# Kernel tuning notes

Hardware: AMD Instinct MI355X
Metric: run time of the kernel (lower is better)

Reference implementation:

```python
import jax, jax.numpy as jnp
import numpy as np

B, L, D, H = 2, 2048, 1024, 16
HD = D // H  # head_dim = 64


def setup_inputs() -> dict:
    key = jax.random.key(0)
    ks = jax.random.split(key, 10)
    s_in = 1.0 / np.sqrt(D)
    x = jax.random.normal(ks[0], (B, L, D), dtype=jnp.float32)
    attn_mask = jnp.ones((B, L), dtype=jnp.int32)
    # Per-head QKV projections stacked along head axis: (H, D, HD)
    Wq = jax.random.normal(ks[1], (H, D, HD), dtype=jnp.float32) * s_in
    bq = jnp.zeros((H, HD), dtype=jnp.float32)
    Wk = jax.random.normal(ks[2], (H, D, HD), dtype=jnp.float32) * s_in
    bk = jnp.zeros((H, HD), dtype=jnp.float32)
    Wv = jax.random.normal(ks[3], (H, D, HD), dtype=jnp.float32) * s_in
    bv = jnp.zeros((H, HD), dtype=jnp.float32)
    # Output projection (D, D)
    Wo = jax.random.normal(ks[4], (D, D), dtype=jnp.float32) * s_in
    bo = jnp.zeros((D,), dtype=jnp.float32)
    return {"x": x, "attn_mask": attn_mask, "Wq": Wq, "bq": bq,
            "Wk": Wk, "bk": bk, "Wv": Wv, "bv": bv, "Wo": Wo, "bo": bo}


def reference(x, attn_mask, Wq, bq, Wk, bk, Wv, bv, Wo, bo):
    # Batched equivalent of the per-head loop: q,k,v -> (B, H, L, HD)
    q = jnp.einsum('bld,hde->bhle', x, Wq) + bq[None, :, None, :]
    k = jnp.einsum('bld,hde->bhle', x, Wk) + bk[None, :, None, :]
    v = jnp.einsum('bld,hde->bhle', x, Wv) + bv[None, :, None, :]
    scale = 1.0 / jnp.sqrt(jnp.asarray(HD, dtype=x.dtype))
    scores = jnp.einsum('bhle,bhme->bhlm', q, k) * scale  # (B, H, L, L)
    # attn_mask (B, L): mask out keys where mask == 0
    neg = jnp.asarray(-1e9, dtype=scores.dtype)
    scores = jnp.where(attn_mask[:, None, None, :] != 0, scores, neg)
    attn = jax.nn.softmax(scores, axis=-1)
    ctx = jnp.einsum('bhlm,bhme->bhle', attn, v)  # (B, H, L, HD)
    # Concatenate heads (head h occupies dims [h*HD:(h+1)*HD]) then project
    concat = jnp.transpose(ctx, (0, 2, 1, 3)).reshape(B, L, D)
    out = jnp.einsum('bld,de->ble', concat, Wo) + bo
    return out
```

## Files before the change

kernel.cpp:

```cpp
#include <hip/hip_runtime.h>

constexpr int Bz = 2, Lz = 2048, Dz = 1024, Hz = 16, HDz = 64;
constexpr int QSZ = Bz * Hz * Lz * HDz;
constexpr int SPLIT = 2;
constexpr int KSPAN = Lz / SPLIT;

typedef __attribute__((ext_vector_type(8))) __bf16 bf16x8;
typedef __attribute__((ext_vector_type(4))) float f32x4;

__device__ __forceinline__ float b2f(unsigned int u) {
    union { float f; unsigned int i; } c; c.i = u << 16; return c.f;
}
__device__ __forceinline__ unsigned short f2b(float x) {
    union { float f; unsigned int u; } c; c.f = x;
    unsigned int u = c.u;
    return (unsigned short)((u + 0x7fffu + ((u >> 16) & 1u)) >> 16);
}
__device__ __forceinline__ void ld8(const float* p, float* f) {
    float4 a = *(const float4*)p, b = *(const float4*)(p + 4);
    f[0] = a.x; f[1] = a.y; f[2] = a.z; f[3] = a.w;
    f[4] = b.x; f[5] = b.y; f[6] = b.z; f[7] = b.w;
}
__device__ __forceinline__ int swb(int row, int e) {
    return row * 64 + ((((e >> 3) ^ row) & 7) << 3) + (e & 7);
}

__global__ void ws_sentinel(float* __restrict__ out) {
    if (threadIdx.x == 0 && blockIdx.x == 0) out[0] = 100.0f;
}

__global__ __launch_bounds__(256) void cvt_x(
    const float* __restrict__ x, unsigned short* __restrict__ xb) {
    int idx = (blockIdx.x * 256 + threadIdx.x) * 8;
    float f[8]; ld8(x + idx, f);
    union { unsigned short s[8]; uint4 u; } o;
    #pragma unroll
    for (int j = 0; j < 8; ++j) o.s[j] = f2b(f[j]);
    *(uint4*)(xb + idx) = o.u;
}

__global__ __launch_bounds__(256) void cvt_w(
    const float* __restrict__ Wq, const float* __restrict__ Wk,
    const float* __restrict__ Wv, const float* __restrict__ Wo,
    unsigned short* __restrict__ Wt, unsigned short* __restrict__ Wot) {
    const int tid = threadIdx.x;
    const int z = blockIdx.z;
    const int kseg = blockIdx.x * 4 + (tid >> 6);
    const int k0 = kseg * 16;
    unsigned short o[16];
    if (z < 3) {
        const float* W = (z == 0) ? Wq : (z == 1) ? Wk : Wv;
        const int h = blockIdx.y, n = tid & 63;
        const float* src = W + (size_t)h * Dz * HDz;
        #pragma unroll
        for (int j = 0; j < 16; ++j) o[j] = f2b(src[(size_t)(k0 + j) * HDz + n]);
        unsigned short* dst = Wt + ((size_t)((z * Hz + h) * HDz) + n) * Dz + k0;
        *(uint4*)dst = *(uint4*)o;
        *(uint4*)(dst + 8) = *(uint4*)(o + 8);
    } else {
        const int n = blockIdx.y * 64 + (tid & 63);
        #pragma unroll
        for (int j = 0; j < 16; ++j) o[j] = f2b(Wo[(size_t)(k0 + j) * Dz + n]);
        unsigned short* dst = Wot + (size_t)n * Dz + k0;
        *(uint4*)dst = *(uint4*)o;
        *(uint4*)(dst + 8) = *(uint4*)(o + 8);
    }
}

__global__ __launch_bounds__(256) void qkv_mfma(
    const unsigned short* __restrict__ xb, const unsigned short* __restrict__ Wt,
    const float* __restrict__ bq, const float* __restrict__ bk,
    const float* __restrict__ bv, unsigned short* __restrict__ qkv) {
    const int l0 = blockIdx.x * 256;
    const int h = blockIdx.y;
    const int which = blockIdx.z % 3;
    const int b = blockIdx.z / 3;
    const float* bias = (which == 0) ? bq : (which == 1) ? bk : bv;
    const int tid = threadIdx.x, wave = tid >> 6, lane = tid & 63;
    const int quad = lane >> 4, l16 = lane & 15;

    __shared__ __align__(16) unsigned short As[256 * 64];
    __shared__ __align__(16) unsigned short Bs[64 * 64];

    const unsigned short* xrow = xb + (size_t)(b * Lz + l0) * Dz;
    const unsigned short* wbase = Wt + (size_t)((which * Hz + h) * HDz) * Dz;

    f32x4 acc[4][4];
    #pragma unroll
    for (int mi = 0; mi < 4; ++mi)
        #pragma unroll
        for (int ni = 0; ni < 4; ++ni) acc[mi][ni] = (f32x4){0.f, 0.f, 0.f, 0.f};

    for (int t = 0; t < Dz / 64; ++t) {
        const int k0 = t * 64;
        #pragma unroll
        for (int i = 0; i < 8; ++i) {
            int ci = tid + i * 256;
            int row = ci >> 3, c = ci & 7;
            uint4 u = *(const uint4*)(xrow + (size_t)row * Dz + k0 + c * 8);
            *(uint4*)&As[row * 64 + ((c ^ (row & 7)) << 3)] = u;
        }
        #pragma unroll
        for (int i = 0; i < 2; ++i) {
            int ci = tid + i * 256;
            int n = ci >> 3, c = ci & 7;
            uint4 u = *(const uint4*)(wbase + (size_t)n * Dz + k0 + c * 8);
            *(uint4*)&Bs[n * 64 + ((c ^ (n & 7)) << 3)] = u;
        }
        __syncthreads();
        #pragma unroll
        for (int kh = 0; kh < 2; ++kh) {
            bf16x8 a[4], bb[4];
            #pragma unroll
            for (int mi = 0; mi < 4; ++mi)
                a[mi] = *(const bf16x8*)&As[swb(wave * 64 + mi * 16 + l16, kh * 32 + quad * 8)];
            #pragma unroll
            for (int ni = 0; ni < 4; ++ni)
                bb[ni] = *(const bf16x8*)&Bs[swb(ni * 16 + l16, kh * 32 + quad * 8)];
            #pragma unroll
            for (int mi = 0; mi < 4; ++mi)
                #pragma unroll
                for (int ni = 0; ni < 4; ++ni)
                    acc[mi][ni] = __builtin_amdgcn_mfma_f32_16x16x32_bf16(
                        a[mi], bb[ni], acc[mi][ni], 0, 0, 0);
        }
        __syncthreads();
    }
    unsigned short* outp = qkv + (size_t)which * QSZ + ((size_t)(b * Hz + h) * Lz + l0) * HDz;
    #pragma unroll
    for (int ni = 0; ni < 4; ++ni) {
        float bvv = bias[h * HDz + ni * 16 + l16];
        #pragma unroll
        for (int mi = 0; mi < 4; ++mi)
            #pragma unroll
            for (int r = 0; r < 4; ++r) {
                int row = wave * 64 + mi * 16 + quad * 4 + r;
                outp[(size_t)row * HDz + ni * 16 + l16] = f2b(acc[mi][ni][r] + bvv);
            }
    }
}

__global__ __launch_bounds__(256) void attn_mfma(
    const unsigned short* __restrict__ qkv, const int* __restrict__ mask,
    unsigned short* __restrict__ Opart, float* __restrict__ lsb) {
    const int b = blockIdx.z >> 1, split = blockIdx.z & 1;
    const int h = blockIdx.y, qb = blockIdx.x;
    const int wave = threadIdx.x >> 6, lane = threadIdx.x & 63;
    const int quad = lane >> 4, l16 = lane & 15;
    const unsigned short* Q = qkv + (size_t)((b * Hz + h) * Lz) * HDz;
    const unsigned short* K = Q + QSZ;
    const unsigned short* V = Q + 2 * (size_t)QSZ;

    __shared__ __align__(16) unsigned short Ks[64 * 64];
    __shared__ __align__(16) unsigned short Vt[64 * 64];
    __shared__ __align__(16) unsigned short Pw[4][32 * 64];

    const int row0 = qb * 128 + wave * 32;
    bf16x8 aq[2][2];
    #pragma unroll
    for (int s = 0; s < 2; ++s) {
        const unsigned short* qp = Q + (size_t)(row0 + s * 16 + l16) * HDz;
        aq[s][0] = *(const bf16x8*)(qp + quad * 8);
        aq[s][1] = *(const bf16x8*)(qp + 32 + quad * 8);
    }

    f32x4 O[2][4];
    #pragma unroll
    for (int s = 0; s < 2; ++s)
        #pragma unroll
        for (int nc = 0; nc < 4; ++nc) O[s][nc] = (f32x4){0.f, 0.f, 0.f, 0.f};
    float lacc[2] = {0.f, 0.f};

    const int vp = threadIdx.x & 31, vc = threadIdx.x >> 5;

    for (int t = 0; t < KSPAN / 64; ++t) {
        const int kt0 = split * KSPAN + t * 64;
        #pragma unroll
        for (int i = 0; i < 2; ++i) {
            int ci = threadIdx.x + i * 256;
            int key = ci >> 3, c = ci & 7;
            uint4 u = *(const uint4*)(K + (size_t)(kt0 + key) * HDz + c * 8);
            *(uint4*)&Ks[key * 64 + ((c ^ (key & 7)) << 3)] = u;
        }
        {
            const unsigned short* vsrc = V + (size_t)(kt0 + 2 * vp) * HDz + vc * 8;
            uint4 u0 = *(const uint4*)vsrc;
            uint4 u1 = *(const uint4*)(vsrc + HDz);
            unsigned short a0[8], a1[8];
            *(uint4*)a0 = u0; *(uint4*)a1 = u1;
            unsigned int* Vt32 = (unsigned int*)Vt;
            #pragma unroll
            for (int j = 0; j < 8; ++j) {
                int row = vc * 8 + j;
                Vt32[row * 32 + ((((vp >> 2) ^ (row & 7)) << 2) + (vp & 3))] =
                    (unsigned int)a0[j] | ((unsigned int)a1[j] << 16);
            }
        }
        unsigned long long bal = __ballot(mask[b * Lz + kt0 + lane] != 0);
        bool allv = (bal == ~0ull);
        __syncthreads();

        float sh[4][4];
        if (allv) {
            #pragma unroll
            for (int kc = 0; kc < 4; ++kc)
                #pragma unroll
                for (int r = 0; r < 4; ++r) sh[kc][r] = -12.0f;
        } else {
            #pragma unroll
            for (int kc = 0; kc < 4; ++kc)
                #pragma unroll
                for (int r = 0; r < 4; ++r)
                    sh[kc][r] = mask[b * Lz + kt0 + kc * 16 + quad * 4 + r] ? -12.0f : -1e9f;
        }

        unsigned short* Pme = Pw[wave];
        #pragma unroll
        for (int kc = 0; kc < 4; ++kc) {
            bf16x8 aK0 = *(const bf16x8*)&Ks[swb(kc * 16 + l16, quad * 8)];
            bf16x8 aK1 = *(const bf16x8*)&Ks[swb(kc * 16 + l16, 32 + quad * 8)];
            #pragma unroll
            for (int s = 0; s < 2; ++s) {
                f32x4 sv = (f32x4){0.f, 0.f, 0.f, 0.f};
                sv = __builtin_amdgcn_mfma_f32_16x16x32_bf16(aK0, aq[s][0], sv, 0, 0, 0);
                sv = __builtin_amdgcn_mfma_f32_16x16x32_bf16(aK1, aq[s][1], sv, 0, 0, 0);
                float p[4];
                #pragma unroll
                for (int r = 0; r < 4; ++r)
                    p[r] = __expf(fmaf(sv[r], 0.125f, sh[kc][r]));
                lacc[s] += (p[0] + p[1]) + (p[2] + p[3]);
                uint2 pk;
                pk.x = (unsigned int)f2b(p[0]) | ((unsigned int)f2b(p[1]) << 16);
                pk.y = (unsigned int)f2b(p[2]) | ((unsigned int)f2b(p[3]) << 16);
                *(uint2*)&Pme[swb(s * 16 + l16, kc * 16 + quad * 4)] = pk;
            }
        }
        #pragma unroll
        for (int kc2 = 0; kc2 < 2; ++kc2) {
            bf16x8 aP0 = *(const bf16x8*)&Pme[swb(l16, kc2 * 32 + quad * 8)];
            bf16x8 aP1 = *(const bf16x8*)&Pme[swb(16 + l16, kc2 * 32 + quad * 8)];
            #pragma unroll
            for (int nc = 0; nc < 4; ++nc) {
                bf16x8 bV = *(const bf16x8*)&Vt[swb(nc * 16 + l16, kc2 * 32 + quad * 8)];
                O[0][nc] = __builtin_amdgcn_mfma_f32_16x16x32_bf16(aP0, bV, O[0][nc], 0, 0, 0);
                O[1][nc] = __builtin_amdgcn_mfma_f32_16x16x32_bf16(aP1, bV, O[1][nc], 0, 0, 0);
            }
        }
        __syncthreads();
    }
    #pragma unroll
    for (int s = 0; s < 2; ++s) {
        lacc[s] += __shfl_xor(lacc[s], 16, 64);
        lacc[s] += __shfl_xor(lacc[s], 32, 64);
    }
    const size_t rowbase = (size_t)(b * Hz + h) * Lz + row0;
    if (quad == 0) {
        atomicAdd(&lsb[rowbase + l16], lacc[0]);
        atomicAdd(&lsb[rowbase + 16 + l16], lacc[1]);
    }
    unsigned short* Os = Opart + (size_t)split * QSZ + rowbase * HDz - (size_t)row0 * HDz
                         + (size_t)row0 * HDz;
    #pragma unroll
    for (int s = 0; s < 2; ++s)
        #pragma unroll
        for (int r = 0; r < 4; ++r) {
            int row = s * 16 + quad * 4 + r;
            #pragma unroll
            for (int nc = 0; nc < 4; ++nc)
                Os[(size_t)row * HDz + nc * 16 + l16] = f2b(O[s][nc][r]);
        }
}

__global__ __launch_bounds__(256) void combine(
    const unsigned short* __restrict__ Opart, const float* __restrict__ lsb,
    unsigned short* __restrict__ ctx) {
    int idx8 = (blockIdx.x * 256 + threadIdx.x) * 8;
    float inv = 1.0f / lsb[idx8 >> 6];
    uint4 u0 = *(const uint4*)(Opart + idx8);
    uint4 u1 = *(const uint4*)(Opart + QSZ + idx8);
    unsigned short a0[8], a1[8], o[8];
    *(uint4*)a0 = u0; *(uint4*)a1 = u1;
    #pragma unroll
    for (int j = 0; j < 8; ++j)
        o[j] = f2b((b2f(a0[j]) + b2f(a1[j])) * inv);
    *(uint4*)(ctx + idx8) = *(uint4*)o;
}

__global__ __launch_bounds__(256) void out_mfma(
    const unsigned short* __restrict__ ctx, const unsigned short* __restrict__ Wot,
    const float* __restrict__ bo, float* __restrict__ out) {
    const int r0 = blockIdx.x * 128;
    const int n0 = blockIdx.y * 64;
    const int b = r0 >> 11, lbase = r0 & 2047;
    const int tid = threadIdx.x, wave = tid >> 6, lane = tid & 63;
    const int quad = lane >> 4, l16 = lane & 15;

    __shared__ __align__(16) unsigned short As[128 * 64];
    __shared__ __align__(16) unsigned short Bs[64 * 64];

    f32x4 acc[2][4];
    #pragma unroll
    for (int mi = 0; mi < 2; ++mi)
        #pragma unroll
        for (int ni = 0; ni < 4; ++ni) acc[mi][ni] = (f32x4){0.f, 0.f, 0.f, 0.f};

    for (int t = 0; t < Hz; ++t) {
        const unsigned short* abase = ctx + ((size_t)(b * Hz + t) * Lz + lbase) * HDz;
        #pragma unroll
        for (int i = 0; i < 4; ++i) {
            int ci = tid + i * 256;
            int row = ci >> 3, c = ci & 7;
            uint4 u = *(const uint4*)(abase + (size_t)row * HDz + c * 8);
            *(uint4*)&As[row * 64 + ((c ^ (row & 7)) << 3)] = u;
        }
        #pragma unroll
        for (int i = 0; i < 2; ++i) {
            int ci = tid + i * 256;
            int n = ci >> 3, c = ci & 7;
            uint4 u = *(const uint4*)(Wot + (size_t)(n0 + n) * Dz + t * 64 + c * 8);
            *(uint4*)&Bs[n * 64 + ((c ^ (n & 7)) << 3)] = u;
        }
        __syncthreads();
        #pragma unroll
        for (int kh = 0; kh < 2; ++kh) {
            bf16x8 a[2], bb[4];
            #pragma unroll
            for (int mi = 0; mi < 2; ++mi)
                a[mi] = *(const bf16x8*)&As[swb(wave * 32 + mi * 16 + l16, kh * 32 + quad * 8)];
            #pragma unroll
            for (int ni = 0; ni < 4; ++ni)
                bb[ni] = *(const bf16x8*)&Bs[swb(ni * 16 + l16, kh * 32 + quad * 8)];
            #pragma unroll
            for (int mi = 0; mi < 2; ++mi)
                #pragma unroll
                for (int ni = 0; ni < 4; ++ni)
                    acc[mi][ni] = __builtin_amdgcn_mfma_f32_16x16x32_bf16(
                        a[mi], bb[ni], acc[mi][ni], 0, 0, 0);
        }
        __syncthreads();
    }
    #pragma unroll
    for (int ni = 0; ni < 4; ++ni) {
        float bvv = bo[n0 + ni * 16 + l16];
        #pragma unroll
        for (int mi = 0; mi < 2; ++mi)
            #pragma unroll
            for (int r = 0; r < 4; ++r) {
                int row = r0 + wave * 32 + mi * 16 + quad * 4 + r;
                out[(size_t)row * Dz + n0 + ni * 16 + l16] = acc[mi][ni][r] + bvv;
            }
    }
}

extern "C" void kernel_launch(void* const* d_in, const int* in_sizes, int n_in,
                              void* d_out, int out_size, void* d_ws, size_t ws_size,
                              hipStream_t stream) {
    const float* x    = (const float*)d_in[0];
    const int*   mask = (const int*)d_in[1];
    const float* Wq = (const float*)d_in[2];
    const float* bq = (const float*)d_in[3];
    const float* Wk = (const float*)d_in[4];
    const float* bk = (const float*)d_in[5];
    const float* Wv = (const float*)d_in[6];
    const float* bv = (const float*)d_in[7];
    const float* Wo = (const float*)d_in[8];
    const float* bo = (const float*)d_in[9];
    float* out = (float*)d_out;

    const size_t WT_E  = (size_t)3 * Hz * HDz * Dz;
    const size_t WOT_E = (size_t)Dz * Dz;
    const size_t LS_E  = (size_t)Bz * Hz * Lz;
    const size_t NEED = 256 + ((size_t)3 * QSZ + WT_E + WOT_E) * sizeof(unsigned short)
                        + LS_E * sizeof(float);
    if (ws_size < NEED) {
        ws_sentinel<<<1, 64, 0, stream>>>(out);
        return;
    }
    unsigned short* qkv = (unsigned short*)((char*)d_ws + 256);
    unsigned short* Wt  = qkv + (size_t)3 * QSZ;
    unsigned short* Wot = Wt + WT_E;
    float* lsb = (float*)(Wot + WOT_E);
    unsigned short* xb    = (unsigned short*)d_out;
    unsigned short* Opart = (unsigned short*)d_out;

    hipMemsetAsync(lsb, 0, LS_E * sizeof(float), stream);
    cvt_x<<<(Bz * Lz * Dz) / (256 * 8), 256, 0, stream>>>(x, xb);
    cvt_w<<<dim3(16, 16, 4), 256, 0, stream>>>(Wq, Wk, Wv, Wo, Wt, Wot);
    qkv_mfma<<<dim3(Lz / 256, Hz, Bz * 3), 256, 0, stream>>>(xb, Wt, bq, bk, bv, qkv);
    attn_mfma<<<dim3(Lz / 128, Hz, Bz * SPLIT), 256, 0, stream>>>(qkv, mask, Opart, lsb);
    combine<<<QSZ / (256 * 8), 256, 0, stream>>>(Opart, lsb, qkv);
    out_mfma<<<dim3((Bz * Lz) / 128, Dz / 64), 256, 0, stream>>>(qkv, Wot, bo, out);
}
```

Measured before the change: 230.0 us.

## Fuse prep kernels, retile QKV GEMM to 128x128, use hardware bf16 packing

Merges the x conversion, weight conversion and lsb memset into a single prep launch to cut launch overhead. Retiles the QKV projection as one GEMM over all 3*H*HD output columns with 128x128 tiles and a 2x2 wave layout, scattering results into the per-head q/k/v layout at store time. This improves operand reuse per tile and changes the grid shape. It also replaces the manual float-to-bf16 rounding with native bf16x2 conversions in several kernels, which may round slightly differently on edge cases.

```diff
diff --git a/kernel.cpp b/kernel.cpp
--- a/kernel.cpp
+++ b/kernel.cpp
@@ -6,6 +6,7 @@
 constexpr int KSPAN = Lz / SPLIT;
 
 typedef __attribute__((ext_vector_type(8))) __bf16 bf16x8;
+typedef __attribute__((ext_vector_type(2))) __bf16 bf16x2;
 typedef __attribute__((ext_vector_type(4))) float f32x4;
 
 __device__ __forceinline__ float b2f(unsigned int u) {
@@ -16,6 +17,11 @@
     unsigned int u = c.u;
     return (unsigned short)((u + 0x7fffu + ((u >> 16) & 1u)) >> 16);
 }
+__device__ __forceinline__ unsigned int pkbf(float a, float b) {
+    union { bf16x2 v; unsigned int u; } c;
+    c.v = (bf16x2){(__bf16)a, (__bf16)b};
+    return c.u;
+}
 __device__ __forceinline__ void ld8(const float* p, float* f) {
     float4 a = *(const float4*)p, b = *(const float4*)(p + 4);
     f[0] = a.x; f[1] = a.y; f[2] = a.z; f[3] = a.w;
@@ -29,41 +35,46 @@
     if (threadIdx.x == 0 && blockIdx.x == 0) out[0] = 100.0f;
 }
 
-__global__ __launch_bounds__(256) void cvt_x(
-    const float* __restrict__ x, unsigned short* __restrict__ xb) {
-    int idx = (blockIdx.x * 256 + threadIdx.x) * 8;
-    float f[8]; ld8(x + idx, f);
-    union { unsigned short s[8]; uint4 u; } o;
-    #pragma unroll
-    for (int j = 0; j < 8; ++j) o.s[j] = f2b(f[j]);
-    *(uint4*)(xb + idx) = o.u;
-}
-
-__global__ __launch_bounds__(256) void cvt_w(
+__global__ __launch_bounds__(256) void prep(
+    const float* __restrict__ x,
     const float* __restrict__ Wq, const float* __restrict__ Wk,
     const float* __restrict__ Wv, const float* __restrict__ Wo,
-    unsigned short* __restrict__ Wt, unsigned short* __restrict__ Wot) {
-    const int tid = threadIdx.x;
-    const int z = blockIdx.z;
-    const int kseg = blockIdx.x * 4 + (tid >> 6);
-    const int k0 = kseg * 16;
-    unsigned short o[16];
-    if (z < 3) {
-        const float* W = (z == 0) ? Wq : (z == 1) ? Wk : Wv;
-        const int h = blockIdx.y, n = tid & 63;
-        const float* src = W + (size_t)h * Dz * HDz;
-        #pragma unroll
-        for (int j = 0; j < 16; ++j) o[j] = f2b(src[(size_t)(k0 + j) * HDz + n]);
-        unsigned short* dst = Wt + ((size_t)((z * Hz + h) * HDz) + n) * Dz + k0;
-        *(uint4*)dst = *(uint4*)o;
-        *(uint4*)(dst + 8) = *(uint4*)(o + 8);
+    unsigned short* __restrict__ xb, unsigned short* __restrict__ Wt,
+    unsigned short* __restrict__ Wot, float* __restrict__ lsb) {
+    const int bid = blockIdx.x, tid = threadIdx.x;
+    if (bid < 2048) {
+        int idx = (bid * 256 + tid) * 8;
+        float f[8]; ld8(x + idx, f);
+        unsigned int o[4];
+        #pragma unroll
+        for (int j = 0; j < 4; ++j) o[j] = pkbf(f[2 * j], f[2 * j + 1]);
+        *(uint4*)(xb + idx) = *(uint4*)o;
+    } else if (bid < 2048 + 1024) {
+        int zz = bid - 2048;
+        int z = zz >> 8, y = (zz >> 4) & 15, xk = zz & 15;
+        int kseg = xk * 4 + (tid >> 6);
+        int k0 = kseg * 16;
+        unsigned short o[16];
+        if (z < 3) {
+            const float* W = (z == 0) ? Wq : (z == 1) ? Wk : Wv;
+            const int h = y, n = tid & 63;
+            const float* src = W + (size_t)h * Dz * HDz;
+            #pragma unroll
+            for (int j = 0; j < 16; ++j) o[j] = f2b(src[(size_t)(k0 + j) * HDz + n]);
+            unsigned short* dst = Wt + ((size_t)((z * Hz + h) * HDz) + n) * Dz + k0;
+            *(uint4*)dst = *(uint4*)o;
+            *(uint4*)(dst + 8) = *(uint4*)(o + 8);
+        } else {
+            const int n = y * 64 + (tid & 63);
+            #pragma unroll
+            for (int j = 0; j < 16; ++j) o[j] = f2b(Wo[(size_t)(k0 + j) * Dz + n]);
+            unsigned short* dst = Wot + (size_t)n * Dz + k0;
+            *(uint4*)dst = *(uint4*)o;
+            *(uint4*)(dst + 8) = *(uint4*)(o + 8);
+        }
     } else {
-        const int n = blockIdx.y * 64 + (tid & 63);
-        #pragma unroll
-        for (int j = 0; j < 16; ++j) o[j] = f2b(Wo[(size_t)(k0 + j) * Dz + n]);
-        unsigned short* dst = Wot + (size_t)n * Dz + k0;
-        *(uint4*)dst = *(uint4*)o;
-        *(uint4*)(dst + 8) = *(uint4*)(o + 8);
+        int i = (bid - 3072) * 1024 + tid * 4;
+        *(float4*)(lsb + i) = (float4){0.f, 0.f, 0.f, 0.f};
     }
 }
 
@@ -71,19 +82,17 @@
     const unsigned short* __restrict__ xb, const unsigned short* __restrict__ Wt,
     const float* __restrict__ bq, const float* __restrict__ bk,
     const float* __restrict__ bv, unsigned short* __restrict__ qkv) {
-    const int l0 = blockIdx.x * 256;
-    const int h = blockIdx.y;
-    const int which = blockIdx.z % 3;
-    const int b = blockIdx.z / 3;
-    const float* bias = (which == 0) ? bq : (which == 1) ? bk : bv;
+    const int rblk = blockIdx.x;
+    const int nblk = blockIdx.y;
     const int tid = threadIdx.x, wave = tid >> 6, lane = tid & 63;
     const int quad = lane >> 4, l16 = lane & 15;
-
-    __shared__ __align__(16) unsigned short As[256 * 64];
-    __shared__ __align__(16) unsigned short Bs[64 * 64];
-
-    const unsigned short* xrow = xb + (size_t)(b * Lz + l0) * Dz;
-    const unsigned short* wbase = Wt + (size_t)((which * Hz + h) * HDz) * Dz;
+    const int wm = wave >> 1, wn = wave & 1;
+
+    __shared__ __align__(16) unsigned short As[128 * 64];
+    __shared__ __align__(16) unsigned short Bs[128 * 64];
+
+    const unsigned short* arow = xb + (size_t)rblk * 128 * Dz;
+    const unsigned short* brow = Wt + (size_t)nblk * 128 * Dz;
 
     f32x4 acc[4][4];
     #pragma unroll
@@ -94,18 +103,18 @@
     for (int t = 0; t < Dz / 64; ++t) {
         const int k0 = t * 64;
         #pragma unroll
-        for (int i = 0; i < 8; ++i) {
+        for (int i = 0; i < 4; ++i) {
             int ci = tid + i * 256;
             int row = ci >> 3, c = ci & 7;
-            uint4 u = *(const uint4*)(xrow + (size_t)row * Dz + k0 + c * 8);
+            uint4 u = *(const uint4*)(arow + (size_t)row * Dz + k0 + c * 8);
             *(uint4*)&As[row * 64 + ((c ^ (row & 7)) << 3)] = u;
         }
         #pragma unroll
-        for (int i = 0; i < 2; ++i) {
+        for (int i = 0; i < 4; ++i) {
             int ci = tid + i * 256;
-            int n = ci >> 3, c = ci & 7;
-            uint4 u = *(const uint4*)(wbase + (size_t)n * Dz + k0 + c * 8);
-            *(uint4*)&Bs[n * 64 + ((c ^ (n & 7)) << 3)] = u;
+            int row = ci >> 3, c = ci & 7;
+            uint4 u = *(const uint4*)(brow + (size_t)row * Dz + k0 + c * 8);
+            *(uint4*)&Bs[row * 64 + ((c ^ (row & 7)) << 3)] = u;
         }
         __syncthreads();
         #pragma unroll
@@ -113,10 +122,10 @@
             bf16x8 a[4], bb[4];
             #pragma unroll
             for (int mi = 0; mi < 4; ++mi)
-                a[mi] = *(const bf16x8*)&As[swb(wave * 64 + mi * 16 + l16, kh * 32 + quad * 8)];
+                a[mi] = *(const bf16x8*)&As[swb(wm * 64 + mi * 16 + l16, kh * 32 + quad * 8)];
             #pragma unroll
             for (int ni = 0; ni < 4; ++ni)
-                bb[ni] = *(const bf16x8*)&Bs[swb(ni * 16 + l16, kh * 32 + quad * 8)];
+                bb[ni] = *(const bf16x8*)&Bs[swb(wn * 64 + ni * 16 + l16, kh * 32 + quad * 8)];
             #pragma unroll
             for (int mi = 0; mi < 4; ++mi)
                 #pragma unroll
@@ -126,16 +135,22 @@
         }
         __syncthreads();
     }
-    unsigned short* outp = qkv + (size_t)which * QSZ + ((size_t)(b * Hz + h) * Lz + l0) * HDz;
+    const int row_base = rblk * 128 + wm * 64;
     #pragma unroll
     for (int ni = 0; ni < 4; ++ni) {
-        float bvv = bias[h * HDz + ni * 16 + l16];
+        int n_base = nblk * 128 + wn * 64 + ni * 16;
+        int which = n_base >> 10, h = (n_base >> 6) & 15, e0 = n_base & 63;
+        const float* bp = (which == 0) ? bq : (which == 1) ? bk : bv;
+        float bval = bp[h * HDz + e0 + l16];
+        unsigned short* base = qkv + (size_t)which * QSZ;
         #pragma unroll
         for (int mi = 0; mi < 4; ++mi)
             #pragma unroll
             for (int r = 0; r < 4; ++r) {
-                int row = wave * 64 + mi * 16 + quad * 4 + r;
-                outp[(size_t)row * HDz + ni * 16 + l16] = f2b(acc[mi][ni][r] + bvv);
+                int row = row_base + mi * 16 + quad * 4 + r;
+                int b_ = row >> 11, l = row & 2047;
+                base[((size_t)(b_ * Hz + h) * Lz + l) * HDz + e0 + l16] =
+                    f2b(acc[mi][ni][r] + bval);
             }
     }
 }
@@ -230,8 +245,8 @@
                     p[r] = __expf(fmaf(sv[r], 0.125f, sh[kc][r]));
                 lacc[s] += (p[0] + p[1]) + (p[2] + p[3]);
                 uint2 pk;
-                pk.x = (unsigned int)f2b(p[0]) | ((unsigned int)f2b(p[1]) << 16);
-                pk.y = (unsigned int)f2b(p[2]) | ((unsigned int)f2b(p[3]) << 16);
+                pk.x = pkbf(p[0], p[1]);
+                pk.y = pkbf(p[2], p[3]);
                 *(uint2*)&Pme[swb(s * 16 + l16, kc * 16 + quad * 4)] = pk;
             }
         }
@@ -258,8 +273,7 @@
         atomicAdd(&lsb[rowbase + l16], lacc[0]);
         atomicAdd(&lsb[rowbase + 16 + l16], lacc[1]);
     }
-    unsigned short* Os = Opart + (size_t)split * QSZ + rowbase * HDz - (size_t)row0 * HDz
-                         + (size_t)row0 * HDz;
+    unsigned short* Os = Opart + (size_t)split * QSZ + rowbase * HDz;
     #pragma unroll
     for (int s = 0; s < 2; ++s)
         #pragma unroll
@@ -278,11 +292,13 @@
     float inv = 1.0f / lsb[idx8 >> 6];
     uint4 u0 = *(const uint4*)(Opart + idx8);
     uint4 u1 = *(const uint4*)(Opart + QSZ + idx8);
-    unsigned short a0[8], a1[8], o[8];
+    unsigned short a0[8], a1[8];
     *(uint4*)a0 = u0; *(uint4*)a1 = u1;
-    #pragma unroll
-    for (int j = 0; j < 8; ++j)
-        o[j] = f2b((b2f(a0[j]) + b2f(a1[j])) * inv);
+    unsigned int o[4];
+    #pragma unroll
+    for (int j = 0; j < 4; ++j)
+        o[j] = pkbf((b2f(a0[2 * j]) + b2f(a1[2 * j])) * inv,
+                    (b2f(a0[2 * j + 1]) + b2f(a1[2 * j + 1])) * inv);
     *(uint4*)(ctx + idx8) = *(uint4*)o;
 }
 
@@ -383,10 +399,8 @@
     unsigned short* xb    = (unsigned short*)d_out;
     unsigned short* Opart = (unsigned short*)d_out;
 
-    hipMemsetAsync(lsb, 0, LS_E * sizeof(float), stream);
-    cvt_x<<<(Bz * Lz * Dz) / (256 * 8), 256, 0, stream>>>(x, xb);
-    cvt_w<<<dim3(16, 16, 4), 256, 0, stream>>>(Wq, Wk, Wv, Wo, Wt, Wot);
-    qkv_mfma<<<dim3(Lz / 256, Hz, Bz * 3), 256, 0, stream>>>(xb, Wt, bq, bk, bv, qkv);
+    prep<<<2048 + 1024 + 64, 256, 0, stream>>>(x, Wq, Wk, Wv, Wo, xb, Wt, Wot, lsb);
+    qkv_mfma<<<dim3(32, 24), 256, 0, stream>>>(xb, Wt, bq, bk, bv, qkv);
     attn_mfma<<<dim3(Lz / 128, Hz, Bz * SPLIT), 256, 0, stream>>>(qkv, mask, Opart, lsb);
     combine<<<QSZ / (256 * 8), 256, 0, stream>>>(Opart, lsb, qkv);
     out_mfma<<<dim3((Bz * Lz) / 128, Dz / 64), 256, 0, stream>>>(qkv, Wot, bo, out);
```

New measurement: 241.6 us. 1.05x slower.
